# Performance work log

Hardware: AMD Instinct MI355X
Metric: run time of the kernel (lower is better)

The kernel has to match this reference:

```python
import jax, jax.numpy as jnp
import numpy as np
from math import sqrt

RELATIVE_CUTOFF = 128
VALUE_DIM = 64


def _skew(m):
    # m: (b, h, S, 2S-1) -> (b, h, S, S), out[i, j] = m[i, j - i + S - 1]
    b, h, S, _ = m.shape
    m = jnp.pad(m, ((0, 0), (0, 0), (0, 0), (0, 1)))          # (b,h,S,2S)
    m = m.reshape(b, h, 2 * S * S)
    m = jnp.pad(m, ((0, 0), (0, 0), (0, S - 1)))
    m = m.reshape(b, h, S + 1, 2 * S - 1)
    return m[:, :, :S, S - 1:]


def setup_inputs() -> dict:
    key = jax.random.key(0)
    ks = jax.random.split(key, 5)
    B, S, E, H, Dk, Dv = 2, 2048, 512, 8, 64, 64
    return {
        "xs": jax.random.normal(ks[0], (B, S, E), dtype=jnp.float32),
        "w_q": jax.random.normal(ks[1], (H, E, Dk), dtype=jnp.float32) * (1.0 / sqrt(E)),
        "w_k": jax.random.normal(ks[2], (H, E, Dk), dtype=jnp.float32) * (1.0 / sqrt(E)),
        "w_v": jax.random.normal(ks[3], (H, E, Dv), dtype=jnp.float32) * (1.0 / sqrt(E)),
        "w_o": jnp.ones((H,), dtype=jnp.float32),
        "a_k": jax.random.normal(ks[4], (2 * RELATIVE_CUTOFF + 1, Dk), dtype=jnp.float32) * 0.1,
    }


def reference(xs, w_q, w_k, w_v, w_o, a_k):
    S = xs.shape[1]
    queries = jnp.einsum("bse,heq->bhsq", xs, w_q)
    keys = jnp.einsum("bse,hek->bhsk", xs, w_k)
    values = jnp.einsum("bse,hev->bhsv", xs, w_v)

    # relative positional embeddings: pos in [-S+1, S-1], clamped to cutoff
    pos = jnp.clip(jnp.arange(-S + 1, S), -RELATIVE_CUTOFF, RELATIVE_CUTOFF) + RELATIVE_CUTOFF
    rel = a_k[pos]                                             # (2S-1, Dk)

    q_k = jnp.einsum("bhiq,bhjq->bhij", queries, keys)
    q_rel = _skew(jnp.einsum("bhiq,rq->bhir", queries, rel))   # (b,h,S,S)

    e = (q_k + q_rel) / sqrt(VALUE_DIM)
    alphas = jax.nn.softmax(e, axis=3)
    z = jnp.einsum("bhij,bhjv->bhiv", alphas, values)
    return jnp.einsum("bhsv,h->bsv", z, w_o)
```

## Files before the change

### kernel.cpp

```cpp
#include <hip/hip_runtime.h>
#include <hip/hip_bf16.h>

#define S_LEN 2048
#define E_DIM 512
#define D_DIM 64
#define H_NUM 8
#define B_NUM 2
#define BH_NUM 16
#define NQA 257
#define QAE_W 512
#define KSPLIT 2
#define KV_PER (S_LEN / KSPLIT)
#define NT (KV_PER / 64)
#define QTILE 256

typedef _Float16 half8 __attribute__((ext_vector_type(8)));
typedef float f32x16 __attribute__((ext_vector_type(16)));
typedef unsigned int uint2v __attribute__((ext_vector_type(2)));
typedef unsigned int uint4v __attribute__((ext_vector_type(4)));

static __device__ __forceinline__ f32x16 MFMA(half8 a, half8 b, f32x16 c) {
    return __builtin_amdgcn_mfma_f32_32x32x16_f16(a, b, c, 0, 0, 0);
}
static __device__ __forceinline__ f32x16 ZERO16() {
    f32x16 z;
    #pragma unroll
    for (int i = 0; i < 16; ++i) z[i] = 0.f;
    return z;
}
static __device__ __forceinline__ unsigned int PKRTZ(float a, float b) {
    return __builtin_bit_cast(unsigned int, __builtin_amdgcn_cvt_pkrtz(a, b));
}

__global__ __launch_bounds__(256) void cast_x_kernel(
    const float* __restrict__ xs, _Float16* __restrict__ Xh)
{
    const int idx = (blockIdx.x * 256 + threadIdx.x) * 8;
    float4 a = *(const float4*)&xs[idx];
    float4 b = *(const float4*)&xs[idx + 4];
    half8 o;
    o[0] = (_Float16)a.x; o[1] = (_Float16)a.y; o[2] = (_Float16)a.z; o[3] = (_Float16)a.w;
    o[4] = (_Float16)b.x; o[5] = (_Float16)b.y; o[6] = (_Float16)b.z; o[7] = (_Float16)b.w;
    *(half8*)&Xh[idx] = o;
}

__global__ __launch_bounds__(256) void cast_wak_kernel(
    const float* __restrict__ w_q, const float* __restrict__ w_k,
    const float* __restrict__ w_v, const float* __restrict__ w_o,
    const float* __restrict__ a_k,
    _Float16* __restrict__ Wht, _Float16* __restrict__ akh)
{
    __shared__ float T[64][68];
    const int type = blockIdx.z;
    const int t = threadIdx.x;
    if (type == 3) {
        const int bn = blockIdx.y * 8 + blockIdx.x;
        if (bn >= 9) return;
        const int idx = (bn * 256 + t) * 8;
        if (idx < NQA * 64) {
            float4 a = *(const float4*)&a_k[idx];
            float4 b = *(const float4*)&a_k[idx + 4];
            half8 o;
            o[0] = (_Float16)a.x; o[1] = (_Float16)a.y; o[2] = (_Float16)a.z; o[3] = (_Float16)a.w;
            o[4] = (_Float16)b.x; o[5] = (_Float16)b.y; o[6] = (_Float16)b.z; o[7] = (_Float16)b.w;
            *(half8*)&akh[idx] = o;
        }
        return;
    }
    const int kt = blockIdx.x, h = blockIdx.y;
    const float* W = (type == 0) ? w_q : (type == 1) ? w_k : w_v;
    const float scale = (type == 0) ? 0.18033688011112042f
                                    : (type == 2 ? w_o[h] : 1.0f);
    const int kr = t >> 2, nseg = (t & 3) * 16;
    #pragma unroll
    for (int i = 0; i < 4; ++i)
        *(float4*)&T[kr][nseg + 4 * i] =
            *(const float4*)&W[((size_t)h * 512 + kt * 64 + kr) * 64 + nseg + 4 * i];
    __syncthreads();
    const int nr = t >> 2, kseg = (t & 3) * 16;
    _Float16* dst = Wht + ((size_t)(type * 8 + h) * 64 + nr) * 512 + kt * 64 + kseg;
    #pragma unroll
    for (int i = 0; i < 2; ++i) {
        half8 o;
        #pragma unroll
        for (int j = 0; j < 8; ++j) o[j] = (_Float16)(T[kseg + 8 * i + j][nr] * scale);
        *(half8*)&dst[8 * i] = o;
    }
}

__global__ __launch_bounds__(256) void proj_mfma_kernel(
    const _Float16* __restrict__ Xh, const _Float16* __restrict__ Wht,
    const _Float16* __restrict__ akh,
    _Float16* __restrict__ Qh, _Float16* __restrict__ Kh,
    _Float16* __restrict__ Vt, _Float16* __restrict__ QAe)
{
    __shared__ __align__(16) _Float16 raw[30208];
    _Float16 (*Xlds)[128][72] = (_Float16(*)[128][72])raw;
    _Float16 (*Wlds)[64][72]  = (_Float16(*)[64][72])(raw + 18432);
    _Float16* ob  = raw;
    _Float16 (*ak)[72] = (_Float16(*)[72])(raw + 9216);
    _Float16* SLo = raw + 29952;
    _Float16* SHi = raw + 30080;

    const int mt = blockIdx.x, bh = blockIdx.y, type = blockIdx.z;
    const int b = bh >> 3, h = bh & 7;
    const int m0 = mt * 128;
    const int t = threadIdx.x, wid = t >> 6, lane = t & 63;
    const int lq = lane & 31, lh = lane >> 5;

    const _Float16* W = Wht + (size_t)(type * 8 + h) * 64 * 512;
    const _Float16* X = Xh + ((size_t)b * S_LEN + m0) * 512;

    const int xrow = t >> 1, xseg = (t & 1) * 32;
    const int wrow = t >> 2, wseg = (t & 3) * 16;

    #pragma unroll
    for (int i = 0; i < 4; ++i)
        *(half8*)&Xlds[0][xrow][xseg + 8 * i] =
            *(const half8*)&X[(size_t)xrow * 512 + xseg + 8 * i];
    #pragma unroll
    for (int i = 0; i < 2; ++i)
        *(half8*)&Wlds[0][wrow][wseg + 8 * i] =
            *(const half8*)&W[(size_t)wrow * 512 + wseg + 8 * i];
    __syncthreads();

    f32x16 acc[2];
    acc[0] = ZERO16(); acc[1] = ZERO16();
    int cur = 0;
    for (int c = 0; c < 8; ++c) {
        half8 xst[4], wst[2];
        if (c < 7) {
            const int k0 = (c + 1) * 64;
            #pragma unroll
            for (int i = 0; i < 4; ++i)
                xst[i] = *(const half8*)&X[(size_t)xrow * 512 + k0 + xseg + 8 * i];
            #pragma unroll
            for (int i = 0; i < 2; ++i)
                wst[i] = *(const half8*)&W[(size_t)wrow * 512 + k0 + wseg + 8 * i];
        }
        #pragma unroll
        for (int kc = 0; kc < 4; ++kc) {
            half8 a  = *(const half8*)&Xlds[cur][wid * 32 + lq][kc * 16 + lh * 8];
            half8 b0 = *(const half8*)&Wlds[cur][lq][kc * 16 + lh * 8];
            half8 b1 = *(const half8*)&Wlds[cur][32 + lq][kc * 16 + lh * 8];
            acc[0] = MFMA(a, b0, acc[0]);
            acc[1] = MFMA(a, b1, acc[1]);
        }
        if (c < 7) {
            #pragma unroll
            for (int i = 0; i < 4; ++i)
                *(half8*)&Xlds[cur ^ 1][xrow][xseg + 8 * i] = xst[i];
            #pragma unroll
            for (int i = 0; i < 2; ++i)
                *(half8*)&Wlds[cur ^ 1][wrow][wseg + 8 * i] = wst[i];
        }
        __syncthreads();
        cur ^= 1;
    }

    #pragma unroll
    for (int n = 0; n < 2; ++n)
        #pragma unroll
        for (int r = 0; r < 16; ++r) {
            int row = wid * 32 + (r & 3) + ((r >> 2) << 3) + (lh << 2);
            ob[row * 72 + n * 32 + lq] = (_Float16)acc[n][r];
        }
    __syncthreads();

    if (type == 2) {
        const int v = t >> 2, sseg = (t & 3) * 32;
        _Float16* dst = Vt + ((size_t)bh * 64 + v) * S_LEN + m0 + sseg;
        #pragma unroll
        for (int i = 0; i < 4; ++i) {
            half8 o;
            #pragma unroll
            for (int j = 0; j < 8; ++j) o[j] = ob[(sseg + 8 * i + j) * 72 + v];
            *(half8*)&dst[8 * i] = o;
        }
        return;
    }

    {
        _Float16* P = (type == 0) ? Qh : Kh;
        const int row = t >> 1, seg = (t & 1) * 32;
        _Float16* dst = P + ((size_t)bh * S_LEN + m0 + row) * 64 + seg;
        #pragma unroll
        for (int i = 0; i < 4; ++i)
            *(half8*)&dst[8 * i] = *(const half8*)&ob[row * 72 + seg + 8 * i];
    }
    if (type != 0) return;

    for (int r = t; r < 288; r += 256) {
        if (r < NQA) {
            #pragma unroll
            for (int i = 0; i < 8; ++i)
                *(half8*)&ak[r][8 * i] = *(const half8*)&akh[(size_t)r * 64 + 8 * i];
        } else {
            half8 z = {};
            #pragma unroll
            for (int i = 0; i < 8; ++i) *(half8*)&ak[r][8 * i] = z;
        }
    }
    __syncthreads();

    half8 qfr[4];
    #pragma unroll
    for (int kc = 0; kc < 4; ++kc)
        qfr[kc] = *(const half8*)&ob[(wid * 32 + lq) * 72 + kc * 16 + lh * 8];

    for (int nsub = 0; nsub < 9; ++nsub) {
        f32x16 qa = ZERO16();
        #pragma unroll
        for (int kc = 0; kc < 4; ++kc) {
            half8 bf = *(const half8*)&ak[nsub * 32 + lq][kc * 16 + lh * 8];
            qa = MFMA(qfr[kc], bf, qa);
        }
        const int col = nsub * 32 + lq;
        if (col < NQA) {
            #pragma unroll
            for (int r = 0; r < 16; ++r) {
                const int row = m0 + wid * 32 + (r & 3) + ((r >> 2) << 3) + (lh << 2);
                const _Float16 v = (_Float16)qa[r];
                QAe[((size_t)bh * S_LEN + row) * QAE_W + col + 128] = v;
                if (col == 0)   SLo[row - m0] = v;
                if (col == 256) SHi[row - m0] = v;
            }
        }
    }
    __syncthreads();

    const int prow = t >> 1, pseg = (t & 1) * 64;
    const _Float16 lo = SLo[prow], hi = SHi[prow];
    half8 vlo, vhi;
    #pragma unroll
    for (int j = 0; j < 8; ++j) { vlo[j] = lo; vhi[j] = hi; }
    _Float16* pb = QAe + ((size_t)bh * S_LEN + m0 + prow) * QAE_W;
    #pragma unroll
    for (int i = 0; i < 8; ++i) {
        *(half8*)&pb[pseg + 8 * i] = vlo;
        *(half8*)&pb[384 + pseg + 8 * i] = vhi;
    }
}

__global__ __launch_bounds__(512) void attn_kernel(
    const _Float16* __restrict__ Qh, const _Float16* __restrict__ Kh,
    const _Float16* __restrict__ Vt, const _Float16* __restrict__ QAe,
    _Float16* __restrict__ Po, float2* __restrict__ Ml)
{
    __shared__ __align__(16) char smraw[36864];
    _Float16 (*Klds)[64][72] = (_Float16(*)[64][72])smraw;
    _Float16 (*Vlds)[64][72] = (_Float16(*)[64][72])(smraw + 18432);
    _Float16* Obuf = (_Float16*)smraw;
    __shared__ __align__(16) _Float16 Bnd[8][32][128];

    const int p0 = blockIdx.x;
    const int nb = (p0 & 7) * 32 + (p0 >> 3);
    const int bh = nb >> 4;
    const int rem = nb & 15;
    const int qt = rem & 7, ks = rem >> 3;
    const int i0 = qt * QTILE, k0 = ks * KV_PER;

    const int t = threadIdx.x, wid = t >> 6, lane = t & 63;
    const int lq = lane & 31, lh = lane >> 5;
    const int i0w = i0 + wid * 32;
    const int qg = i0w + lq;

    int mode = 0;
    if (k0 >= i0 + QTILE - 1 + 128) mode = 1;
    else if (k0 + KV_PER - 1 <= i0 - 128) mode = 2;

    half8 qf[4];
    #pragma unroll
    for (int kc = 0; kc < 4; ++kc)
        qf[kc] = *(const half8*)&Qh[((size_t)bh * S_LEN + qg) * 64 + kc * 16 + lh * 8];

    const _Float16* qaeRow = QAe + ((size_t)bh * S_LEN + qg) * QAE_W;
    const float qa_lo = (float)qaeRow[128];
    const float qa_hi = (float)qaeRow[384];
    const _Float16* BndSrc = QAe + ((size_t)bh * S_LEN + i0w) * QAE_W;

    float rm = -1e30f, rl = 0.f;
    f32x16 acco[2];
    acco[0] = ZERO16(); acco[1] = ZERO16();

    const int srow = t >> 3, sseg = (t & 7) * 8;
    const _Float16* Kbase = Kh + ((size_t)bh * S_LEN + k0) * 64;
    const _Float16* Vbase = Vt + ((size_t)bh * 64 + srow) * S_LEN + k0;

    const int brow = lane >> 4;
    const int bcol = (lane & 15) * 8;

    half8 kst, vst, breg[8];
    *(half8*)&Klds[0][srow][sseg] = *(const half8*)&Kbase[(size_t)srow * 64 + sseg];
    *(half8*)&Vlds[0][srow][sseg] = *(const half8*)&Vbase[sseg];
    kst = *(const half8*)&Kbase[(size_t)(64 + srow) * 64 + sseg];
    vst = *(const half8*)&Vbase[64 + sseg];

    bool inb_next;
    {
        const int d0 = k0 - i0w;
        inb_next = (mode == 0) && (d0 < 159) && (d0 > -191);
        if (inb_next) {
            const int cw0n = (d0 + 225) & ~7;
            #pragma unroll
            for (int ps = 0; ps < 8; ++ps)
                breg[ps] = *(const half8*)&BndSrc[(size_t)(ps * 4 + brow) * QAE_W + cw0n + bcol];
        }
    }
    __syncthreads();

    for (int jt = 0; jt < NT; ++jt) {
        const int cur = jt & 1;
        if (jt) __syncthreads();
        if (jt + 1 < NT) {
            *(half8*)&Klds[cur ^ 1][srow][sseg] = kst;
            *(half8*)&Vlds[cur ^ 1][srow][sseg] = vst;
        }
        if (jt + 2 < NT) {
            const int jg = (jt + 2) * 64;
            kst = *(const half8*)&Kbase[(size_t)(jg + srow) * 64 + sseg];
            vst = *(const half8*)&Vbase[jg + sseg];
        }

        const int diff = k0 + jt * 64 - i0w;
        const bool inband = inb_next;
        const int cw0 = (diff + 225) & ~7;

        if (inband) {
            #pragma unroll
            for (int ps = 0; ps < 8; ++ps)
                *(half8*)&Bnd[wid][ps * 4 + brow][bcol] = breg[ps];
        }
        {
            const int dn = diff + 64;
            inb_next = (jt + 1 < NT) && (mode == 0) && (dn < 159) && (dn > -191);
            if (inb_next) {
                const int cw0n = (dn + 225) & ~7;
                #pragma unroll
                for (int ps = 0; ps < 8; ++ps)
                    breg[ps] = *(const half8*)&BndSrc[(size_t)(ps * 4 + brow) * QAE_W + cw0n + bcol];
            }
        }

        f32x16 accs[2];
        accs[0] = ZERO16(); accs[1] = ZERO16();
        __builtin_amdgcn_s_setprio(1);
        #pragma unroll
        for (int kc = 0; kc < 4; ++kc) {
            half8 ka = *(const half8*)&Klds[cur][lq][kc * 16 + lh * 8];
            half8 kb = *(const half8*)&Klds[cur][32 + lq][kc * 16 + lh * 8];
            accs[0] = MFMA(ka, qf[kc], accs[0]);
            accs[1] = MFMA(kb, qf[kc], accs[1]);
        }
        __builtin_amdgcn_s_setprio(0);

        const bool allhi = (mode == 1) || (mode == 0 && diff >= 159);
        const bool alllo = (mode == 2) || (mode == 0 && diff <= -191);
        float bunif = 0.f;
        if (allhi) bunif = qa_hi;
        else if (alllo) bunif = qa_lo;
        else {
            asm volatile("s_waitcnt lgkmcnt(0)" ::: "memory");
            __builtin_amdgcn_sched_barrier(0);
            const int pb = diff + 256 - cw0 - lq;
            #pragma unroll
            for (int m = 0; m < 2; ++m)
                #pragma unroll
                for (int r = 0; r < 16; ++r) {
                    const int keyoff = m * 32 + (r & 3) + ((r >> 2) << 3) + (lh << 2);
                    accs[m][r] += (float)Bnd[wid][lq][pb + keyoff];
                }
        }

        float t8[8];
        #pragma unroll
        for (int i = 0; i < 8; ++i)
            t8[i] = fmaxf(fmaxf(accs[0][i], accs[0][i + 8]),
                          fmaxf(accs[1][i], accs[1][i + 8]));
        float tmax = fmaxf(fmaxf(fmaxf(t8[0], t8[1]), fmaxf(t8[2], t8[3])),
                           fmaxf(fmaxf(t8[4], t8[5]), fmaxf(t8[6], t8[7])));
        tmax = fmaxf(tmax, __shfl_xor(tmax, 32));
        const float mnew = fmaxf(rm, tmax + bunif);
        const bool resc = __any(mnew > rm);
        const float corr = exp2f(rm - mnew);
        const float shift = mnew - bunif;
        rm = mnew;

        #pragma unroll
        for (int m = 0; m < 2; ++m)
            #pragma unroll
            for (int r = 0; r < 16; ++r)
                accs[m][r] = exp2f(accs[m][r] - shift);

        float s8[8];
        #pragma unroll
        for (int i = 0; i < 8; ++i)
            s8[i] = (accs[0][i] + accs[0][i + 8]) + (accs[1][i] + accs[1][i + 8]);
        float psum = ((s8[0] + s8[1]) + (s8[2] + s8[3])) +
                     ((s8[4] + s8[5]) + (s8[6] + s8[7]));
        psum += __shfl_xor(psum, 32);

        if (resc) {
            rl = rl * corr + psum;
            #pragma unroll
            for (int n = 0; n < 2; ++n)
                #pragma unroll
                for (int r = 0; r < 16; ++r) acco[n][r] *= corr;
        } else {
            rl += psum;
        }

        half8 pf[4];
        #pragma unroll
        for (int kc = 0; kc < 4; ++kc) {
            const int m = kc >> 1, rb = (kc & 1) * 8;
            unsigned int a01 = PKRTZ(accs[m][rb + 0], accs[m][rb + 1]);
            unsigned int a45 = PKRTZ(accs[m][rb + 4], accs[m][rb + 5]);
            unsigned int a23 = PKRTZ(accs[m][rb + 2], accs[m][rb + 3]);
            unsigned int a67 = PKRTZ(accs[m][rb + 6], accs[m][rb + 7]);
            uint2v r02 = __builtin_amdgcn_permlane32_swap(a01, a45, false, false);
            uint2v r13 = __builtin_amdgcn_permlane32_swap(a23, a67, false, false);
            uint4v wv;
            wv[0] = r02[0]; wv[1] = r13[0]; wv[2] = r02[1]; wv[3] = r13[1];
            pf[kc] = __builtin_bit_cast(half8, wv);
        }

        __builtin_amdgcn_s_setprio(1);
        #pragma unroll
        for (int kc = 0; kc < 4; ++kc) {
            half8 v0 = *(const half8*)&Vlds[cur][lq][kc * 16 + lh * 8];
            half8 v1 = *(const half8*)&Vlds[cur][32 + lq][kc * 16 + lh * 8];
            acco[0] = MFMA(v0, pf[kc], acco[0]);
            acco[1] = MFMA(v1, pf[kc], acco[1]);
        }
        __builtin_amdgcn_s_setprio(0);
    }

    __syncthreads();
    const int orow = wid * 32 + lq;
    #pragma unroll
    for (int n = 0; n < 2; ++n)
        #pragma unroll
        for (int rq = 0; rq < 4; ++rq) {
            uint2v hv;
            hv[0] = PKRTZ(acco[n][rq * 4 + 0], acco[n][rq * 4 + 1]);
            hv[1] = PKRTZ(acco[n][rq * 4 + 2], acco[n][rq * 4 + 3]);
            *(uint2v*)&Obuf[(size_t)orow * 72 + n * 32 + rq * 8 + lh * 4] = hv;
        }
    if (lh == 0)
        Ml[((size_t)ks * BH_NUM + bh) * S_LEN + qg] = make_float2(rm, rl);
    asm volatile("s_waitcnt lgkmcnt(0)" ::: "memory");
    __builtin_amdgcn_sched_barrier(0);
    const int rrow = wid * 32 + (lane >> 1);
    const int rseg = (lane & 1) * 32;
    _Float16* dst = Po + (((size_t)ks * BH_NUM + bh) * S_LEN + i0 + rrow) * 64 + rseg;
    #pragma unroll
    for (int i = 0; i < 4; ++i)
        *(half8*)&dst[8 * i] = *(const half8*)&Obuf[(size_t)rrow * 72 + rseg + 8 * i];
}

__global__ __launch_bounds__(256) void merge_kernel(
    const _Float16* __restrict__ Po, const float2* __restrict__ Ml,
    float* __restrict__ out)
{
    const int b = blockIdx.y;
    const int s = blockIdx.x * 32 + (threadIdx.x >> 3);
    const int v0 = (threadIdx.x & 7) * 8;
    float acc[8] = {0, 0, 0, 0, 0, 0, 0, 0};
    #pragma unroll
    for (int h = 0; h < 8; ++h) {
        const int bh = b * 8 + h;
        float m[KSPLIT], l[KSPLIT];
        #pragma unroll
        for (int p = 0; p < KSPLIT; ++p) {
            const float2 v = Ml[((size_t)p * BH_NUM + bh) * S_LEN + s];
            m[p] = v.x; l[p] = v.y;
        }
        float M = fmaxf(m[0], m[1]);
        float L = 0.f, w[KSPLIT];
        #pragma unroll
        for (int p = 0; p < KSPLIT; ++p) { w[p] = exp2f(m[p] - M); L += w[p] * l[p]; }
        const float invL = 1.0f / L;
        #pragma unroll
        for (int p = 0; p < KSPLIT; ++p) {
            half8 o = *(const half8*)&Po[(((size_t)p * BH_NUM + bh) * S_LEN + s) * 64 + v0];
            const float wp = w[p] * invL;
            #pragma unroll
            for (int j = 0; j < 8; ++j) acc[j] += wp * (float)o[j];
        }
    }
    float4 o0 = {acc[0], acc[1], acc[2], acc[3]};
    float4 o1 = {acc[4], acc[5], acc[6], acc[7]};
    *(float4*)&out[((size_t)b * S_LEN + s) * 64 + v0] = o0;
    *(float4*)&out[((size_t)b * S_LEN + s) * 64 + v0 + 4] = o1;
}

extern "C" void kernel_launch(void* const* d_in, const int* in_sizes, int n_in,
                              void* d_out, int out_size, void* d_ws, size_t ws_size,
                              hipStream_t stream)
{
    const float* xs  = (const float*)d_in[0];
    const float* w_q = (const float*)d_in[1];
    const float* w_k = (const float*)d_in[2];
    const float* w_v = (const float*)d_in[3];
    const float* w_o = (const float*)d_in[4];
    const float* a_k = (const float*)d_in[5];
    float* out = (float*)d_out;

    char* w = (char*)d_ws;
    _Float16* Xh  = (_Float16*)w;  w += (size_t)B_NUM * S_LEN * E_DIM * 2;
    _Float16* Wht = (_Float16*)w;  w += (size_t)3 * H_NUM * 64 * 512 * 2;
    _Float16* akh = (_Float16*)w;  w += 33024;
    _Float16* Qh  = (_Float16*)w;  w += (size_t)BH_NUM * S_LEN * 64 * 2;
    _Float16* Kh  = (_Float16*)w;  w += (size_t)BH_NUM * S_LEN * 64 * 2;
    _Float16* Vt  = (_Float16*)w;  w += (size_t)BH_NUM * S_LEN * 64 * 2;
    _Float16* QAe = (_Float16*)w;  w += (size_t)BH_NUM * S_LEN * QAE_W * 2;
    _Float16* Po  = (_Float16*)w;  w += (size_t)KSPLIT * BH_NUM * S_LEN * 64 * 2;
    float2*   Ml  = (float2*)w;

    cast_x_kernel<<<1024, 256, 0, stream>>>(xs, Xh);
    cast_wak_kernel<<<dim3(8, 8, 4), 256, 0, stream>>>(w_q, w_k, w_v, w_o, a_k, Wht, akh);
    proj_mfma_kernel<<<dim3(16, 16, 3), 256, 0, stream>>>(Xh, Wht, akh, Qh, Kh, Vt, QAe);
    attn_kernel<<<256, 512, 0, stream>>>(Qh, Kh, Vt, QAe, Po, Ml);
    merge_kernel<<<dim3(64, 2), 256, 0, stream>>>(Po, Ml, out);
}
```

Before: 89.94 us.

## Interleave KV tiles across splits and switch softmax to natural exp

The two KV splits no longer take contiguous halves of the key range. Each split now takes alternating 64-key tiles, so every block sees a similar share of the relative-position band tiles, which are the expensive ones. This removes the per-block mode shortcut and is meant to balance work across blocks. The Q prescale also drops the log2(e) factor and the exponentials use __expf instead of exp2f, which may add a multiply per element.

```diff
diff --git a/kernel.cpp b/kernel.cpp
--- a/kernel.cpp
+++ b/kernel.cpp
@@ -10,8 +10,7 @@
 #define NQA 257
 #define QAE_W 512
 #define KSPLIT 2
-#define KV_PER (S_LEN / KSPLIT)
-#define NT (KV_PER / 64)
+#define NT (S_LEN / KSPLIT / 64)
 #define QTILE 256
 
 typedef _Float16 half8 __attribute__((ext_vector_type(8)));
@@ -69,8 +68,7 @@
     }
     const int kt = blockIdx.x, h = blockIdx.y;
     const float* W = (type == 0) ? w_q : (type == 1) ? w_k : w_v;
-    const float scale = (type == 0) ? 0.18033688011112042f
-                                    : (type == 2 ? w_o[h] : 1.0f);
+    const float scale = (type == 0) ? 0.125f : (type == 2 ? w_o[h] : 1.0f);
     const int kr = t >> 2, nseg = (t & 3) * 16;
     #pragma unroll
     for (int i = 0; i < 4; ++i)
@@ -258,17 +256,13 @@
     const int bh = nb >> 4;
     const int rem = nb & 15;
     const int qt = rem & 7, ks = rem >> 3;
-    const int i0 = qt * QTILE, k0 = ks * KV_PER;
+    const int i0 = qt * QTILE;
 
     const int t = threadIdx.x, wid = t >> 6, lane = t & 63;
     const int lq = lane & 31, lh = lane >> 5;
     const int i0w = i0 + wid * 32;
     const int qg = i0w + lq;
 
-    int mode = 0;
-    if (k0 >= i0 + QTILE - 1 + 128) mode = 1;
-    else if (k0 + KV_PER - 1 <= i0 - 128) mode = 2;
-
     half8 qf[4];
     #pragma unroll
     for (int kc = 0; kc < 4; ++kc)
@@ -284,22 +278,23 @@
     acco[0] = ZERO16(); acco[1] = ZERO16();
 
     const int srow = t >> 3, sseg = (t & 7) * 8;
-    const _Float16* Kbase = Kh + ((size_t)bh * S_LEN + k0) * 64;
-    const _Float16* Vbase = Vt + ((size_t)bh * 64 + srow) * S_LEN + k0;
+    const _Float16* Kbase = Kh + (size_t)bh * S_LEN * 64;
+    const _Float16* Vbase = Vt + ((size_t)bh * 64 + srow) * S_LEN;
 
     const int brow = lane >> 4;
     const int bcol = (lane & 15) * 8;
 
     half8 kst, vst, breg[8];
-    *(half8*)&Klds[0][srow][sseg] = *(const half8*)&Kbase[(size_t)srow * 64 + sseg];
-    *(half8*)&Vlds[0][srow][sseg] = *(const half8*)&Vbase[sseg];
-    kst = *(const half8*)&Kbase[(size_t)(64 + srow) * 64 + sseg];
-    vst = *(const half8*)&Vbase[64 + sseg];
+    const int kv0 = ks * 64;
+    *(half8*)&Klds[0][srow][sseg] = *(const half8*)&Kbase[(size_t)(kv0 + srow) * 64 + sseg];
+    *(half8*)&Vlds[0][srow][sseg] = *(const half8*)&Vbase[kv0 + sseg];
+    kst = *(const half8*)&Kbase[(size_t)(kv0 + 128 + srow) * 64 + sseg];
+    vst = *(const half8*)&Vbase[kv0 + 128 + sseg];
 
     bool inb_next;
     {
-        const int d0 = k0 - i0w;
-        inb_next = (mode == 0) && (d0 < 159) && (d0 > -191);
+        const int d0 = kv0 - i0w;
+        inb_next = (d0 < 159) && (d0 > -191);
         if (inb_next) {
             const int cw0n = (d0 + 225) & ~7;
             #pragma unroll
@@ -317,12 +312,12 @@
             *(half8*)&Vlds[cur ^ 1][srow][sseg] = vst;
         }
         if (jt + 2 < NT) {
-            const int jg = (jt + 2) * 64;
+            const int jg = kv0 + (jt + 2) * 128;
             kst = *(const half8*)&Kbase[(size_t)(jg + srow) * 64 + sseg];
             vst = *(const half8*)&Vbase[jg + sseg];
         }
 
-        const int diff = k0 + jt * 64 - i0w;
+        const int diff = kv0 + jt * 128 - i0w;
         const bool inband = inb_next;
         const int cw0 = (diff + 225) & ~7;
 
@@ -332,8 +327,8 @@
                 *(half8*)&Bnd[wid][ps * 4 + brow][bcol] = breg[ps];
         }
         {
-            const int dn = diff + 64;
-            inb_next = (jt + 1 < NT) && (mode == 0) && (dn < 159) && (dn > -191);
+            const int dn = diff + 128;
+            inb_next = (jt + 1 < NT) && (dn < 159) && (dn > -191);
             if (inb_next) {
                 const int cw0n = (dn + 225) & ~7;
                 #pragma unroll
@@ -354,8 +349,8 @@
         }
         __builtin_amdgcn_s_setprio(0);
 
-        const bool allhi = (mode == 1) || (mode == 0 && diff >= 159);
-        const bool alllo = (mode == 2) || (mode == 0 && diff <= -191);
+        const bool allhi = (diff >= 159);
+        const bool alllo = (diff <= -191);
         float bunif = 0.f;
         if (allhi) bunif = qa_hi;
         else if (alllo) bunif = qa_lo;
@@ -382,7 +377,7 @@
         tmax = fmaxf(tmax, __shfl_xor(tmax, 32));
         const float mnew = fmaxf(rm, tmax + bunif);
         const bool resc = __any(mnew > rm);
-        const float corr = exp2f(rm - mnew);
+        const float corr = __expf(rm - mnew);
         const float shift = mnew - bunif;
         rm = mnew;
 
@@ -390,7 +385,7 @@
         for (int m = 0; m < 2; ++m)
             #pragma unroll
             for (int r = 0; r < 16; ++r)
-                accs[m][r] = exp2f(accs[m][r] - shift);
+                accs[m][r] = __expf(accs[m][r] - shift);
 
         float s8[8];
         #pragma unroll
@@ -479,7 +474,7 @@
         float M = fmaxf(m[0], m[1]);
         float L = 0.f, w[KSPLIT];
         #pragma unroll
-        for (int p = 0; p < KSPLIT; ++p) { w[p] = exp2f(m[p] - M); L += w[p] * l[p]; }
+        for (int p = 0; p < KSPLIT; ++p) { w[p] = __expf(m[p] - M); L += w[p] * l[p]; }
         const float invL = 1.0f / L;
         #pragma unroll
         for (int p = 0; p < KSPLIT; ++p) {
```

Result: faster. 80.06 us (-11.0%).
